# Performance work log

Hardware: AMD Instinct MI355X
Metric: run time of the kernel (lower is better)

The kernel has to match this reference:

```python
import jax, jax.numpy as jnp
import numpy as np

B, T, D_MODEL, H, RPR_K = 2, 2048, 1024, 16, 8
DK = D_MODEL // H  # 64
NUM_RPR = 2 * RPR_K + 1


def setup_inputs() -> dict:
    key = jax.random.key(0)
    ks = jax.random.split(key, 16)
    s = 0.02
    inp = {
        "query": jax.random.normal(ks[0], (B, T, D_MODEL), jnp.float32),
        "key": jax.random.normal(ks[1], (B, T, D_MODEL), jnp.float32),
        "value": jax.random.normal(ks[2], (B, T, D_MODEL), jnp.float32),
        "mask": jnp.ones((B, 1, 1, T), dtype=bool),
        "w_q": jax.random.normal(ks[3], (D_MODEL, H * DK), jnp.float32) * s,
        "b_q": jnp.zeros((H * DK,), jnp.float32),
        "w_k": jax.random.normal(ks[4], (D_MODEL, H * DK), jnp.float32) * s,
        "b_k": jnp.zeros((H * DK,), jnp.float32),
        "w_v": jax.random.normal(ks[5], (D_MODEL, H * DK), jnp.float32) * s,
        "b_v": jnp.zeros((H * DK,), jnp.float32),
        "w_o": jax.random.normal(ks[6], (H * DK, D_MODEL), jnp.float32) * s,
        "b_o": jnp.zeros((D_MODEL,), jnp.float32),
        "rpr_key_table": jax.random.normal(ks[7], (NUM_RPR, DK), jnp.float32),
        "rpr_value_table": jax.random.normal(ks[8], (NUM_RPR, DK), jnp.float32),
    }
    return inp


def _rel_edges(seq_len):
    # edges[i, j] = clamp(j - i + rpr_k, 0, 2*rpr_k)  -> [T, T] int32
    seq = jnp.arange(seq_len)
    edges = seq[None, :] - seq[:, None] + RPR_K
    return jnp.clip(edges, 0, 2 * RPR_K)


def reference(query, key, value, mask, w_q, b_q, w_k, b_k, w_v, b_v,
              w_o, b_o, rpr_key_table, rpr_value_table):
    Bsz, Tlen, _ = query.shape
    edges = _rel_edges(Tlen)                       # [T, T]
    ek = rpr_key_table[edges]                      # [T, T, DK]
    ev = rpr_value_table[edges]                    # [T, T, DK]

    def proj(x, w, b):
        return (x @ w + b).reshape(Bsz, Tlen, H, DK).transpose(0, 2, 1, 3)  # [B,H,T,DK]

    q = proj(query, w_q, b_q)
    k = proj(key, w_k, b_k)
    v = proj(value, w_v, b_v)

    scores_qk = jnp.einsum('bhtd,bhsd->bhts', q, k)
    scores_qek = jnp.einsum('bhtd,tsd->bhts', q, ek)
    scores = (scores_qk + scores_qek) / jnp.sqrt(jnp.float32(DK))
    scores = jnp.where(mask, scores, jnp.float32(-1e9))
    a = jax.nn.softmax(scores, axis=-1)            # [B,H,T,T]

    upd = jnp.einsum('bhts,bhsd->bhtd', a, v)
    upd_e = jnp.einsum('bhts,tsd->bhtd', a, ev)
    x = (upd + upd_e).transpose(0, 2, 1, 3).reshape(Bsz, Tlen, H * DK)
    return x @ w_o + b_o
```

## Files before the change

### kernel.cpp

```cpp
#include <hip/hip_runtime.h>
#include <stdint.h>


typedef unsigned short u16;
typedef __attribute__((ext_vector_type(4))) float f32x4;
typedef __attribute__((ext_vector_type(16))) float f32x16;
typedef __attribute__((ext_vector_type(4))) int   i32x4;
typedef __attribute__((ext_vector_type(8))) __bf16 bh8;

#define T_LEN 2048
#define NHEAD 16
#define NR    17

#define SCALE_LOG2 0.18033688011112042f

#define AW15_OFF 0
#define LA_OFF   1048576
#define A0_OFF   1114112
#define A16_OFF  1179648
#define LB_OFF   1245184

__device__ __forceinline__ float bf2f(u16 x) {
  unsigned u = ((unsigned)x) << 16;
  return __builtin_bit_cast(float, u);
}
__device__ __forceinline__ u16 f2bf(float f) {
  unsigned u = __builtin_bit_cast(unsigned, f);
  u = u + 0x7fffu + ((u >> 16) & 1u);
  return (u16)(u >> 16);
}
__device__ __forceinline__ f32x4 zero4() { f32x4 z = {0.f, 0.f, 0.f, 0.f}; return z; }
__device__ __forceinline__ f32x16 zero16() {
  f32x16 z = {0.f, 0.f, 0.f, 0.f, 0.f, 0.f, 0.f, 0.f,
              0.f, 0.f, 0.f, 0.f, 0.f, 0.f, 0.f, 0.f};
  return z;
}

__device__ __forceinline__ f32x4 mfma16(bh8 a, bh8 b, f32x4 c) {
  return __builtin_amdgcn_mfma_f32_16x16x32_bf16(a, b, c, 0, 0, 0);
}
__device__ __forceinline__ f32x16 mfma32(bh8 a, bh8 b, f32x16 c) {
  return __builtin_amdgcn_mfma_f32_32x32x16_bf16(a, b, c, 0, 0, 0);
}

__device__ __forceinline__ unsigned cvtpk(float a, float b) {
  unsigned r;
  asm("v_cvt_pk_bf16_f32 %0, %1, %2" : "=v"(r) : "v"(a), "v"(b));
  return r;
}

__device__ __forceinline__ void bar_sync() {
  __builtin_amdgcn_sched_barrier(0);
  asm volatile("s_waitcnt lgkmcnt(0)" ::: "memory");
  __builtin_amdgcn_s_barrier();
  __builtin_amdgcn_sched_barrier(0);
}

__device__ __forceinline__ void wait_vm0() {
  __builtin_amdgcn_sched_barrier(0);
  asm volatile("s_waitcnt vmcnt(0)" ::: "memory");
  __builtin_amdgcn_sched_barrier(0);
}

__device__ __forceinline__ void async16(const u16* g, u16* l) {
  __builtin_amdgcn_global_load_lds(
      (const __attribute__((address_space(1))) void*)g,
      (__attribute__((address_space(3))) void*)l, 16, 0, 0);
}

__device__ __forceinline__ bh8 ldfrag(const u16* base, int row, int qc) {
  const i32x4 v = *(const i32x4*)(base + row * 64 + ((qc ^ (row & 7)) << 3));
  return __builtin_bit_cast(bh8, v);
}

__global__ __launch_bounds__(256) void prep_kernel(
    const float* __restrict__ xq, const float* __restrict__ xk,
    const float* __restrict__ xv, const float* __restrict__ w0,
    const float* __restrict__ w1, const float* __restrict__ w2,
    const float* __restrict__ w3, u16* __restrict__ oq, u16* __restrict__ ok,
    u16* __restrict__ ov, u16* __restrict__ t0, u16* __restrict__ t1,
    u16* __restrict__ t2, u16* __restrict__ t3) {
  __shared__ u16 tile[32][33];
  const int z = blockIdx.z;
  if (z < 3) {
    const float* S = (z == 0) ? xq : (z == 1) ? xk : xv;
    u16* D = (z == 0) ? oq : (z == 1) ? ok : ov;
    const size_t i = ((size_t)blockIdx.x * 256 + threadIdx.x) * 8;
    const f32x4 v0 = *(const f32x4*)(S + i);
    const f32x4 v1 = *(const f32x4*)(S + i + 4);
    u16 o[8];
#pragma unroll
    for (int j = 0; j < 4; ++j) {
      o[j] = f2bf(v0[j]);
      o[4 + j] = f2bf(v1[j]);
    }
    i32x4 w;
    __builtin_memcpy(&w, o, 16);
    *(i32x4*)(D + i) = w;
  } else {
    if (blockIdx.x >= 1024) return;
    const float* S = (z == 3) ? w0 : (z == 4) ? w1 : (z == 5) ? w2 : w3;
    u16* D = (z == 3) ? t0 : (z == 4) ? t1 : (z == 5) ? t2 : t3;
    const int tx = threadIdx.x & 31, ty = threadIdx.x >> 5;
    const int bx = blockIdx.x & 31, by = blockIdx.x >> 5;
#pragma unroll
    for (int i = 0; i < 4; ++i) {
      const int y = by * 32 + ty + i * 8;
      tile[ty + i * 8][tx] = f2bf(S[(size_t)y * 1024 + bx * 32 + tx]);
    }
    __syncthreads();
#pragma unroll
    for (int i = 0; i < 4; ++i) {
      const int y = bx * 32 + ty + i * 8;
      D[(size_t)y * 1024 + by * 32 + tx] = tile[tx][ty + i * 8];
    }
  }
}

__device__ __forceinline__ void gemm_body(const u16* __restrict__ A,
                                          const u16* __restrict__ Bm,
                                          const float* __restrict__ bias,
                                          void* __restrict__ out, int mode,
                                          int bm, int bn, float oscale) {
  __shared__ __align__(16) u16 As[2][128 * 32];
  __shared__ __align__(16) u16 Bs[2][128 * 32];
  const int tid = threadIdx.x;
  const int wv = tid >> 6;
  const int ln = tid & 63;
  const int quad = ln >> 4, l15 = ln & 15;
  const int wr = wv >> 1, wc = wv & 1;

  f32x4 acc[4][4];
#pragma unroll
  for (int i = 0; i < 4; ++i)
#pragma unroll
    for (int j = 0; j < 4; ++j) acc[i][j] = zero4();

  const int c0 = tid, c1 = tid + 256;
  const size_t aoff0 = (size_t)(bm * 128 + (c0 >> 2)) * 1024 + (c0 & 3) * 8;
  const size_t aoff1 = (size_t)(bm * 128 + (c1 >> 2)) * 1024 + (c1 & 3) * 8;
  const size_t boff0 = (size_t)(bn * 128 + (c0 >> 2)) * 1024 + (c0 & 3) * 8;
  const size_t boff1 = (size_t)(bn * 128 + (c1 >> 2)) * 1024 + (c1 & 3) * 8;

  u16* ad0[2] = {&As[0][(wv * 64) * 8], &As[1][(wv * 64) * 8]};
  u16* ad1[2] = {&As[0][(256 + wv * 64) * 8], &As[1][(256 + wv * 64) * 8]};
  u16* bd0[2] = {&Bs[0][(wv * 64) * 8], &Bs[1][(wv * 64) * 8]};
  u16* bd1[2] = {&Bs[0][(256 + wv * 64) * 8], &Bs[1][(256 + wv * 64) * 8]};

  async16(A + aoff0, ad0[0]);
  async16(A + aoff1, ad1[0]);
  async16(Bm + boff0, bd0[0]);
  async16(Bm + boff1, bd1[0]);
  __syncthreads();

  for (int kt = 0; kt < 32; ++kt) {
    const int cur = kt & 1, nxt = cur ^ 1;
    if (kt < 31) {
      const int ko = (kt + 1) * 32;
      async16(A + aoff0 + ko, ad0[nxt]);
      async16(A + aoff1 + ko, ad1[nxt]);
      async16(Bm + boff0 + ko, bd0[nxt]);
      async16(Bm + boff1 + ko, bd1[nxt]);
    }

    bh8 af[4], bf[4];
#pragma unroll
    for (int mi = 0; mi < 4; ++mi)
      af[mi] = __builtin_bit_cast(
          bh8,
          *(const i32x4*)&As[cur][(wr * 64 + mi * 16 + l15) * 32 + quad * 8]);
#pragma unroll
    for (int ni = 0; ni < 4; ++ni)
      bf[ni] = __builtin_bit_cast(
          bh8,
          *(const i32x4*)&Bs[cur][(wc * 64 + ni * 16 + l15) * 32 + quad * 8]);
#pragma unroll
    for (int mi = 0; mi < 4; ++mi)
#pragma unroll
      for (int ni = 0; ni < 4; ++ni)
        acc[mi][ni] = mfma16(af[mi], bf[ni], acc[mi][ni]);

    __syncthreads();
  }

#pragma unroll
  for (int mi = 0; mi < 4; ++mi) {
    const int row0 = bm * 128 + wr * 64 + mi * 16 + quad * 4;
#pragma unroll
    for (int ni = 0; ni < 4; ++ni) {
      const int col = bn * 128 + wc * 64 + ni * 16 + l15;
      const float bcol = (mode == 3) ? 0.f : bias[col];
#pragma unroll
      for (int reg = 0; reg < 4; ++reg) {
        const int r = row0 + reg;
        const float v = acc[mi][ni][reg] + ((mode == 3) ? bias[r] : bcol);
        if (mode == 1) {
          const int bb = r >> 11, t = r & 2047;
          const int h = col >> 6, d = col & 63;
          ((u16*)out)[(((size_t)bb * NHEAD + h) * T_LEN + (size_t)t) * 64 + d] =
              f2bf(v * oscale);
        } else {
          const int h = r >> 6, d = r & 63;
          const int bb = col >> 11, t = col & 2047;
          ((u16*)out)[(((size_t)bb * NHEAD + h) * 64 + (size_t)d) * T_LEN + t] =
              f2bf(v);
        }
      }
    }
  }
}

__global__ __launch_bounds__(256) void gemm_qkv_kernel(
    const u16* __restrict__ xq, const u16* __restrict__ xk,
    const u16* __restrict__ xv, const u16* __restrict__ wtq,
    const u16* __restrict__ wtk, const u16* __restrict__ wtv,
    const float* __restrict__ bq, const float* __restrict__ bk,
    const float* __restrict__ bv, u16* __restrict__ oq, u16* __restrict__ ok,
    u16* __restrict__ ovt) {
  const int z = blockIdx.z;
  if (z == 0)
    gemm_body(xq, wtq, bq, oq, 1, blockIdx.x, blockIdx.y, SCALE_LOG2);
  else if (z == 1)
    gemm_body(xk, wtk, bk, ok, 1, blockIdx.x, blockIdx.y, 1.f);
  else
    gemm_body(wtv, xv, bv, ovt, 3, blockIdx.y, blockIdx.x, 1.f);
}

__global__ __launch_bounds__(256) void gemm_o_kernel(const u16* __restrict__ Ublk,
                                                     const u16* __restrict__ Bm,
                                                     const float* __restrict__ bias,
                                                     float* __restrict__ out) {
  __shared__ __align__(16) u16 As[2][64 * 32];
  __shared__ __align__(16) u16 Bs[2][128 * 32];
  const int tid = threadIdx.x;
  const int wv = tid >> 6;
  const int ln = tid & 63;
  const int quad = ln >> 4, l15 = ln & 15;
  const int wr = wv >> 1, wc = wv & 1;
  const int bm = blockIdx.x, bn = blockIdx.y;

  f32x4 acc[2][4];
#pragma unroll
  for (int i = 0; i < 2; ++i)
#pragma unroll
    for (int j = 0; j < 4; ++j) acc[i][j] = zero4();

  const int c0 = tid, c1 = tid + 256;
  const int rA = bm * 64 + (c0 >> 2);
  const int tA = rA & 2047, bbA = rA >> 11;
  const size_t abase = (size_t)(tA >> 7);
  const size_t boff0 = (size_t)(bn * 128 + (c0 >> 2)) * 1024 + (c0 & 3) * 8;
  const size_t boff1 = (size_t)(bn * 128 + (c1 >> 2)) * 1024 + (c1 & 3) * 8;

  u16* ad0[2] = {&As[0][(wv * 64) * 8], &As[1][(wv * 64) * 8]};
  u16* bd0[2] = {&Bs[0][(wv * 64) * 8], &Bs[1][(wv * 64) * 8]};
  u16* bd1[2] = {&Bs[0][(256 + wv * 64) * 8], &Bs[1][(256 + wv * 64) * 8]};

  auto aoff = [&](int kt) -> size_t {
    const int c = kt * 32 + (c0 & 3) * 8;
    const int h = c >> 6, d = c & 63;
    const size_t idx = (size_t)(bbA * 16 + h) * 16 + abase;
    return idx * 16384 + (size_t)(tA & 127) * 64 + d;
  };

  async16(Ublk + aoff(0), ad0[0]);
  async16(Bm + boff0, bd0[0]);
  async16(Bm + boff1, bd1[0]);
  __syncthreads();

  for (int kt = 0; kt < 32; ++kt) {
    const int cur = kt & 1, nxt = cur ^ 1;
    if (kt < 31) {
      const int ko = (kt + 1) * 32;
      async16(Ublk + aoff(kt + 1), ad0[nxt]);
      async16(Bm + boff0 + ko, bd0[nxt]);
      async16(Bm + boff1 + ko, bd1[nxt]);
    }

    bh8 af[2], bf[4];
#pragma unroll
    for (int mi = 0; mi < 2; ++mi)
      af[mi] = __builtin_bit_cast(
          bh8,
          *(const i32x4*)&As[cur][(wr * 32 + mi * 16 + l15) * 32 + quad * 8]);
#pragma unroll
    for (int ni = 0; ni < 4; ++ni)
      bf[ni] = __builtin_bit_cast(
          bh8,
          *(const i32x4*)&Bs[cur][(wc * 64 + ni * 16 + l15) * 32 + quad * 8]);
#pragma unroll
    for (int mi = 0; mi < 2; ++mi)
#pragma unroll
      for (int ni = 0; ni < 4; ++ni)
        acc[mi][ni] = mfma16(af[mi], bf[ni], acc[mi][ni]);

    __syncthreads();
  }

#pragma unroll
  for (int mi = 0; mi < 2; ++mi) {
    const int row0 = bm * 64 + wr * 32 + mi * 16 + quad * 4;
#pragma unroll
    for (int ni = 0; ni < 4; ++ni) {
      const int col = bn * 128 + wc * 64 + ni * 16 + l15;
      const float bcol = bias[col];
#pragma unroll
      for (int reg = 0; reg < 4; ++reg)
        out[(size_t)(row0 + reg) * 1024 + col] = acc[mi][ni][reg] + bcol;
    }
  }
}

__global__ __launch_bounds__(256, 3) void attn_kernel(
    const u16* __restrict__ Qw, const u16* __restrict__ Kw,
    const u16* __restrict__ Vtw, const float* __restrict__ rkt,
    float* __restrict__ Oa, float* __restrict__ ObLo, float* __restrict__ ObHi,
    float* __restrict__ awb) {
  __shared__ __align__(16) u16 smu[16384];
  __shared__ float smf[4096];
  u16* const Qs = smu;
  float* const qes = smf;
  float* const aw15 = smf + 2176;

  const int tid = threadIdx.x;
  const int wv = tid >> 6, ln = tid & 63;
  const int l31 = ln & 31, hi = ln >> 5;
  const int wg = blockIdx.x;
  const int xcd = wg & 7;
  const int rest = wg >> 3;
  const int sh = rest >> 6;
  const int sub = rest & 63;
  const int qt = sub & 15;
  const int bh = xcd * 4 + (sub >> 4);
  const int idx = bh * 16 + qt;
  const size_t hb = (size_t)bh * (T_LEN * 64);
  const int t0 = qt * 128 + wv * 32;
  const int tl = wv * 32 + l31;

  const int cut = (2 * qt + 3 > 32) ? 32 : (2 * qt + 3);
  const int stBeg = sh ? cut : 0;
  const int stEnd = sh ? 32 : cut;

  float* const opart = (sh == 0)
                           ? (Oa + (size_t)idx * 8192)
                           : (idx < 256 ? ObLo + (size_t)idx * 8192
                                        : ObHi + (size_t)(idx - 256) * 8192);

  if (stBeg >= stEnd) {
    for (int i = tid; i < 8192; i += 256) opart[i] = 0.f;
    if (tid < 128) awb[LB_OFF + idx * 128 + tid] = 0.f;
    return;
  }

  const int r8 = ln >> 3, c8 = ln & 7;
  const int kgp = c8 ^ (r8 & 7);
  const u16* ksrc0 = Kw + hb + (size_t)(wv * 16 + r8) * 64 + kgp * 8;
  const u16* ksrc1 = Kw + hb + (size_t)(wv * 16 + 8 + r8) * 64 + kgp * 8;
  const u16* vsrc0 = Vtw + hb + (size_t)(wv * 16 + r8) * T_LEN + kgp * 8;
  const u16* vsrc1 = Vtw + hb + (size_t)(wv * 16 + 8 + r8) * T_LEN + kgp * 8;
  u16* const ldsK0 = smu + (wv * 16) * 64;
  u16* const ldsK1 = smu + (wv * 16 + 8) * 64;
  u16* const ldsV0 = smu + 8192 + (wv * 16) * 64;
  u16* const ldsV1 = smu + 8192 + (wv * 16 + 8) * 64;

  {
    const u16* qsrc = Qw + hb + (size_t)(qt * 128 + wv * 32 + r8) * 64 + kgp * 8;
#pragma unroll
    for (int a = 0; a < 4; ++a)
      async16(qsrc + (size_t)(a * 8) * 64, Qs + (wv * 32 + a * 8) * 64);
  }
  wait_vm0();
  bar_sync();

  if (sh == 0) {
    for (int i = tid; i < 128 * NR; i += 256) {
      const int row = i / NR, r = i - row * NR;
      float s = 0.f;
#pragma unroll
      for (int c = 0; c < 8; ++c) {
        const i32x4 qv = *(const i32x4*)&Qs[row * 64 + ((c ^ (row & 7)) << 3)];
        const u16* qq = (const u16*)&qv;
#pragma unroll
        for (int j = 0; j < 8; ++j) s += bf2f(qq[j]) * rkt[r * 64 + c * 8 + j];
      }
      qes[i] = s;
    }
    for (int i = tid; i < 128 * 15; i += 256) aw15[i] = 0.f;
  } else {
    for (int row = tid; row < 128; row += 256) {
      float s = 0.f;
#pragma unroll
      for (int c = 0; c < 8; ++c) {
        const i32x4 qv = *(const i32x4*)&Qs[row * 64 + ((c ^ (row & 7)) << 3)];
        const u16* qq = (const u16*)&qv;
#pragma unroll
        for (int j = 0; j < 8; ++j)
          s += bf2f(qq[j]) * rkt[16 * 64 + c * 8 + j];
      }
      qes[row * NR + 16] = s;
    }
  }
  bar_sync();

  const float qb0 = (sh == 0) ? qes[tl * NR + 0] : 0.f;
  const float qb16 = qes[tl * NR + 16];
  bh8 qf[4];
#pragma unroll
  for (int kb = 0; kb < 4; ++kb) qf[kb] = ldfrag(Qs, tl, kb * 2 + hi);
  bar_sync();

  {
    const int b0 = stBeg & 1;
    async16(ksrc0 + (size_t)stBeg * 4096, ldsK0 + b0 * 4096);
    async16(ksrc1 + (size_t)stBeg * 4096, ldsK1 + b0 * 4096);
    async16(vsrc0 + (size_t)stBeg * 64, ldsV0 + b0 * 4096);
    async16(vsrc1 + (size_t)stBeg * 64, ldsV1 + b0 * 4096);
  }
  wait_vm0();
  bar_sync();

  float l_l = 0.f, s0_l = 0.f, s16_l = 0.f;
  f32x16 oacc[2] = {zero16(), zero16()};

  for (int st = stBeg; st < stEnd; ++st) {
    const int cur = st & 1;
    const u16* Kc = smu + cur * 4096;
    const u16* Vc = smu + 8192 + cur * 4096;
    if (st + 1 < stEnd) {
      const int nxt = cur ^ 1;
      async16(ksrc0 + (size_t)(st + 1) * 4096, ldsK0 + nxt * 4096);
      async16(ksrc1 + (size_t)(st + 1) * 4096, ldsK1 + nxt * 4096);
      async16(vsrc0 + (size_t)(st + 1) * 64, ldsV0 + nxt * 4096);
      async16(vsrc1 + (size_t)(st + 1) * 64, ldsV1 + nxt * 4096);
    }
    __builtin_amdgcn_s_setprio(1);

#pragma unroll
    for (int sb = 0; sb < 2; ++sb) {
      f32x16 sacc = zero16();
#pragma unroll
      for (int kb = 0; kb < 4; ++kb) {
        const bh8 kf = ldfrag(Kc, sb * 32 + l31, kb * 2 + hi);
        sacc = mfma32(kf, qf[kb], sacc);
      }

      const int sbase = st * 64 + sb * 32;
      float p[16];
      if (sbase + 39 <= t0) {
        float ts = 0.f;
#pragma unroll
        for (int r = 0; r < 16; ++r) {
          const float pv = __builtin_amdgcn_exp2f(sacc[r] + qb0);
          p[r] = pv;
          ts += pv;
        }
        l_l += ts;
        s0_l += ts;
      } else if (sbase >= t0 + 39) {
        float ts = 0.f;
#pragma unroll
        for (int r = 0; r < 16; ++r) {
          const float pv = __builtin_amdgcn_exp2f(sacc[r] + qb16);
          p[r] = pv;
          ts += pv;
        }
        l_l += ts;
        s16_l += ts;
      } else {
        const int base = sbase + 4 * hi - (t0 + l31) + 8;
#pragma unroll
        for (int r = 0; r < 16; ++r) {
          int rel = base + (r & 3) + 8 * (r >> 2);
          rel = rel < 0 ? 0 : (rel > 16 ? 16 : rel);
          const float pv =
              __builtin_amdgcn_exp2f(sacc[r] + qes[tl * NR + rel]);
          p[r] = pv;
          l_l += pv;
          if (rel == 0)
            s0_l += pv;
          else if (rel == 16)
            s16_l += pv;
          else
            atomicAdd(&aw15[tl * 15 + rel - 1], pv);
        }
      }

#pragma unroll
      for (int h = 0; h < 2; ++h) {
        unsigned wa = cvtpk(p[8 * h + 0], p[8 * h + 1]);
        unsigned wb = cvtpk(p[8 * h + 2], p[8 * h + 3]);
        unsigned wc = cvtpk(p[8 * h + 4], p[8 * h + 5]);
        unsigned wd = cvtpk(p[8 * h + 6], p[8 * h + 7]);
        asm("v_permlane32_swap_b32 %0, %1" : "+v"(wa), "+v"(wc));
        asm("v_permlane32_swap_b32 %0, %1" : "+v"(wb), "+v"(wd));
        const i32x4 fr = {(int)wa, (int)wb, (int)wc, (int)wd};
        const bh8 pa = __builtin_bit_cast(bh8, fr);
        const int ks = sb * 2 + h;
#pragma unroll
        for (int db = 0; db < 2; ++db) {
          const bh8 vf = ldfrag(Vc, db * 32 + l31, ks * 2 + hi);
          oacc[db] = mfma32(pa, vf, oacc[db]);
        }
      }
    }
    __builtin_amdgcn_s_setprio(0);

    wait_vm0();
    bar_sync();
  }

  l_l += __shfl_xor(l_l, 32);
  s0_l += __shfl_xor(s0_l, 32);
  s16_l += __shfl_xor(s16_l, 32);
  if (sh == 0) {
    if (ln < 32) {
      awb[LA_OFF + idx * 128 + tl] = l_l;
      awb[A0_OFF + idx * 128 + tl] = s0_l;
      awb[A16_OFF + idx * 128 + tl] = s16_l;
    }
  } else {
    if (ln < 32) awb[LB_OFF + idx * 128 + tl] = l_l;
  }

#pragma unroll
  for (int r = 0; r < 16; ++r) {
    const int srow = (r & 3) + 8 * (r >> 2) + 4 * hi;
    const int trow = wv * 32 + srow;
    opart[trow * 64 + l31] = oacc[0][r];
    opart[trow * 64 + 32 + l31] = oacc[1][r];
  }

  if (sh == 0) {
    __syncthreads();
    for (int i = tid; i < 128 * 15; i += 256)
      awb[AW15_OFF + (size_t)idx * 1920 + i] = aw15[i];
  }
}

__global__ __launch_bounds__(256) void combine_kernel(
    const float* __restrict__ Oa, const float* __restrict__ ObLo,
    const float* __restrict__ ObHi, const float* __restrict__ awb,
    const float* __restrict__ rvt, u16* __restrict__ Ublk) {
  __shared__ float os[8192];
  __shared__ float rvs[NR * 64];
  const int tid = threadIdx.x;
  const int idx = blockIdx.x;
  const float* oa = Oa + (size_t)idx * 8192;
  const float* ob = (idx < 256) ? ObLo + (size_t)idx * 8192
                                : ObHi + (size_t)(idx - 256) * 8192;
  for (int i = tid; i < 8192; i += 256) os[i] = oa[i] + ob[i];
  for (int i = tid; i < NR * 64; i += 256) rvs[i] = rvt[i];
  __syncthreads();

  const int row = tid >> 1, d0 = (tid & 1) * 32;
  const float lB = awb[LB_OFF + idx * 128 + row];
  const float linv = 1.f / (awb[LA_OFF + idx * 128 + row] + lB);
  const float a0 = awb[A0_OFF + idx * 128 + row];
  const float a16 = awb[A16_OFF + idx * 128 + row] + lB;
  float aw[15];
#pragma unroll
  for (int r = 0; r < 15; ++r)
    aw[r] = awb[AW15_OFF + (size_t)idx * 1920 + row * 15 + r];

#pragma unroll 4
  for (int j = 0; j < 32; ++j) {
    const int d = d0 + j;
    float e = a0 * rvs[d] + a16 * rvs[16 * 64 + d];
#pragma unroll
    for (int r = 1; r < 16; ++r) e += aw[r - 1] * rvs[r * 64 + d];
    const float u = (os[row * 64 + d] + e) * linv;
    Ublk[(size_t)idx * 16384 + row * 64 + d] = f2bf(u);
  }
}

extern "C" void kernel_launch(void* const* d_in, const int* in_sizes, int n_in,
                              void* d_out, int out_size, void* d_ws,
                              size_t ws_size, hipStream_t stream) {
  const float* query = (const float*)d_in[0];
  const float* key = (const float*)d_in[1];
  const float* value = (const float*)d_in[2];
  const float* w_q = (const float*)d_in[4];
  const float* b_q = (const float*)d_in[5];
  const float* w_k = (const float*)d_in[6];
  const float* b_k = (const float*)d_in[7];
  const float* w_v = (const float*)d_in[8];
  const float* b_v = (const float*)d_in[9];
  const float* w_o = (const float*)d_in[10];
  const float* b_o = (const float*)d_in[11];
  const float* rkt = (const float*)d_in[12];
  const float* rvt = (const float*)d_in[13];

  char* ws = (char*)d_ws;
  const size_t MB = 1u << 20;
  u16* wtq = (u16*)(ws + 0 * MB);
  u16* wtk = (u16*)(ws + 2 * MB);
  u16* wtv = (u16*)(ws + 4 * MB);
  u16* wto = (u16*)(ws + 6 * MB);
  u16* Xq = (u16*)(ws + 8 * MB);
  u16* Xk = (u16*)(ws + 16 * MB);
  u16* Xv = (u16*)(ws + 24 * MB);
  u16* Qw = (u16*)(ws + 32 * MB);
  u16* Kw = (u16*)(ws + 40 * MB);
  u16* Vtw = (u16*)(ws + 48 * MB);
  u16* Uw = (u16*)(ws + 56 * MB);
  float* Oa = (float*)(ws + 8 * MB);
  float* ObLo = (float*)(ws + 24 * MB);
  float* ObHi = (float*)(ws + 56 * MB);
  float* awb = (float*)(ws + 0 * MB);
  u16* Ublk = (u16*)(ws + 8 * MB);

  prep_kernel<<<dim3(2048, 1, 7), 256, 0, stream>>>(
      query, key, value, w_q, w_k, w_v, w_o, Xq, Xk, Xv, wtq, wtk, wtv, wto);
  gemm_qkv_kernel<<<dim3(32, 8, 3), 256, 0, stream>>>(
      Xq, Xk, Xv, wtq, wtk, wtv, b_q, b_k, b_v, Qw, Kw, Vtw);
  attn_kernel<<<dim3(1024), 256, 0, stream>>>(Qw, Kw, Vtw, rkt, Oa, ObLo,
                                              ObHi, awb);
  combine_kernel<<<dim3(512), 256, 0, stream>>>(Oa, ObLo, ObHi, awb, rvt,
                                                Ublk);
  gemm_o_kernel<<<dim3(64, 8), 256, 0, stream>>>(Ublk, wto, b_o,
                                                 (float*)d_out);
}
```

Baseline: 282.4 us.

## Split attention KV range evenly and reduce partials with atomics

Attention work is now split into two equal halves of the key range per query tile instead of an uneven causal-style cut, and the partial outputs and band weights are combined with atomicAdd into a zeroed buffer rather than separate per-half buffers. Combine reads one accumulator and writes U in row-major token layout, so gemm_o can use plain strided A loads. The QKV and output GEMM grids are remapped to 1D with XCD-aware tile ordering for better L2 locality. This adds two memsets and atomic traffic, and the second half now recomputes all rpr-key dot products.

Result: slower. 323.7 us (+14.6%).

```diff
diff --git a/kernel.cpp b/kernel.cpp
--- a/kernel.cpp
+++ b/kernel.cpp
@@ -14,11 +14,10 @@
 
 #define SCALE_LOG2 0.18033688011112042f
 
-#define AW15_OFF 0
-#define LA_OFF   1048576
-#define A0_OFF   1114112
-#define A16_OFF  1179648
-#define LB_OFF   1245184
+#define AW15G_OFF 0
+#define LBASE     1048576
+#define A0BASE    1179648
+#define A16BASE   1310720
 
 __device__ __forceinline__ float bf2f(u16 x) {
   unsigned u = ((unsigned)x) << 16;
@@ -217,16 +216,19 @@
     const float* __restrict__ bq, const float* __restrict__ bk,
     const float* __restrict__ bv, u16* __restrict__ oq, u16* __restrict__ ok,
     u16* __restrict__ ovt) {
-  const int z = blockIdx.z;
+  const int wg = blockIdx.x;
+  const int xcd = wg & 7, bn = (wg >> 3) & 7, bmh = (wg >> 6) & 3;
+  const int z = wg >> 8;
+  const int bm = bmh * 8 + xcd;
   if (z == 0)
-    gemm_body(xq, wtq, bq, oq, 1, blockIdx.x, blockIdx.y, SCALE_LOG2);
+    gemm_body(xq, wtq, bq, oq, 1, bm, bn, SCALE_LOG2);
   else if (z == 1)
-    gemm_body(xk, wtk, bk, ok, 1, blockIdx.x, blockIdx.y, 1.f);
+    gemm_body(xk, wtk, bk, ok, 1, bm, bn, 1.f);
   else
-    gemm_body(wtv, xv, bv, ovt, 3, blockIdx.y, blockIdx.x, 1.f);
-}
-
-__global__ __launch_bounds__(256) void gemm_o_kernel(const u16* __restrict__ Ublk,
+    gemm_body(wtv, xv, bv, ovt, 3, bn, bm, 1.f);
+}
+
+__global__ __launch_bounds__(256) void gemm_o_kernel(const u16* __restrict__ A,
                                                      const u16* __restrict__ Bm,
                                                      const float* __restrict__ bias,
                                                      float* __restrict__ out) {
@@ -237,7 +239,9 @@
   const int ln = tid & 63;
   const int quad = ln >> 4, l15 = ln & 15;
   const int wr = wv >> 1, wc = wv & 1;
-  const int bm = blockIdx.x, bn = blockIdx.y;
+  const int wg = blockIdx.x;
+  const int xcd = wg & 7, bn = (wg >> 3) & 7, bmh = wg >> 6;
+  const int bm = bmh * 8 + xcd;
 
   f32x4 acc[2][4];
 #pragma unroll
@@ -246,9 +250,7 @@
     for (int j = 0; j < 4; ++j) acc[i][j] = zero4();
 
   const int c0 = tid, c1 = tid + 256;
-  const int rA = bm * 64 + (c0 >> 2);
-  const int tA = rA & 2047, bbA = rA >> 11;
-  const size_t abase = (size_t)(tA >> 7);
+  const size_t aoff0 = (size_t)(bm * 64 + (c0 >> 2)) * 1024 + (c0 & 3) * 8;
   const size_t boff0 = (size_t)(bn * 128 + (c0 >> 2)) * 1024 + (c0 & 3) * 8;
   const size_t boff1 = (size_t)(bn * 128 + (c1 >> 2)) * 1024 + (c1 & 3) * 8;
 
@@ -256,14 +258,7 @@
   u16* bd0[2] = {&Bs[0][(wv * 64) * 8], &Bs[1][(wv * 64) * 8]};
   u16* bd1[2] = {&Bs[0][(256 + wv * 64) * 8], &Bs[1][(256 + wv * 64) * 8]};
 
-  auto aoff = [&](int kt) -> size_t {
-    const int c = kt * 32 + (c0 & 3) * 8;
-    const int h = c >> 6, d = c & 63;
-    const size_t idx = (size_t)(bbA * 16 + h) * 16 + abase;
-    return idx * 16384 + (size_t)(tA & 127) * 64 + d;
-  };
-
-  async16(Ublk + aoff(0), ad0[0]);
+  async16(A + aoff0, ad0[0]);
   async16(Bm + boff0, bd0[0]);
   async16(Bm + boff1, bd1[0]);
   __syncthreads();
@@ -272,7 +267,7 @@
     const int cur = kt & 1, nxt = cur ^ 1;
     if (kt < 31) {
       const int ko = (kt + 1) * 32;
-      async16(Ublk + aoff(kt + 1), ad0[nxt]);
+      async16(A + aoff0 + ko, ad0[nxt]);
       async16(Bm + boff0 + ko, bd0[nxt]);
       async16(Bm + boff1 + ko, bd1[nxt]);
     }
@@ -314,8 +309,7 @@
 __global__ __launch_bounds__(256, 3) void attn_kernel(
     const u16* __restrict__ Qw, const u16* __restrict__ Kw,
     const u16* __restrict__ Vtw, const float* __restrict__ rkt,
-    float* __restrict__ Oa, float* __restrict__ ObLo, float* __restrict__ ObHi,
-    float* __restrict__ awb) {
+    float* __restrict__ Oacc, float* __restrict__ awb) {
   __shared__ __align__(16) u16 smu[16384];
   __shared__ float smf[4096];
   u16* const Qs = smu;
@@ -327,30 +321,16 @@
   const int l31 = ln & 31, hi = ln >> 5;
   const int wg = blockIdx.x;
   const int xcd = wg & 7;
-  const int rest = wg >> 3;
-  const int sh = rest >> 6;
-  const int sub = rest & 63;
-  const int qt = sub & 15;
-  const int bh = xcd * 4 + (sub >> 4);
+  const int qt = (wg >> 3) & 15;
+  const int bhl = (wg >> 7) & 3;
+  const int sh = wg >> 9;
+  const int bh = xcd * 4 + bhl;
   const int idx = bh * 16 + qt;
   const size_t hb = (size_t)bh * (T_LEN * 64);
   const int t0 = qt * 128 + wv * 32;
   const int tl = wv * 32 + l31;
 
-  const int cut = (2 * qt + 3 > 32) ? 32 : (2 * qt + 3);
-  const int stBeg = sh ? cut : 0;
-  const int stEnd = sh ? 32 : cut;
-
-  float* const opart = (sh == 0)
-                           ? (Oa + (size_t)idx * 8192)
-                           : (idx < 256 ? ObLo + (size_t)idx * 8192
-                                        : ObHi + (size_t)(idx - 256) * 8192);
-
-  if (stBeg >= stEnd) {
-    for (int i = tid; i < 8192; i += 256) opart[i] = 0.f;
-    if (tid < 128) awb[LB_OFF + idx * 128 + tid] = 0.f;
-    return;
-  }
+  const int stBeg = sh * 16, stEnd = stBeg + 16;
 
   const int r8 = ln >> 3, c8 = ln & 7;
   const int kgp = c8 ^ (r8 & 7);
@@ -372,37 +352,22 @@
   wait_vm0();
   bar_sync();
 
-  if (sh == 0) {
-    for (int i = tid; i < 128 * NR; i += 256) {
-      const int row = i / NR, r = i - row * NR;
-      float s = 0.f;
-#pragma unroll
-      for (int c = 0; c < 8; ++c) {
-        const i32x4 qv = *(const i32x4*)&Qs[row * 64 + ((c ^ (row & 7)) << 3)];
-        const u16* qq = (const u16*)&qv;
-#pragma unroll
-        for (int j = 0; j < 8; ++j) s += bf2f(qq[j]) * rkt[r * 64 + c * 8 + j];
-      }
-      qes[i] = s;
-    }
-    for (int i = tid; i < 128 * 15; i += 256) aw15[i] = 0.f;
-  } else {
-    for (int row = tid; row < 128; row += 256) {
-      float s = 0.f;
-#pragma unroll
-      for (int c = 0; c < 8; ++c) {
-        const i32x4 qv = *(const i32x4*)&Qs[row * 64 + ((c ^ (row & 7)) << 3)];
-        const u16* qq = (const u16*)&qv;
-#pragma unroll
-        for (int j = 0; j < 8; ++j)
-          s += bf2f(qq[j]) * rkt[16 * 64 + c * 8 + j];
-      }
-      qes[row * NR + 16] = s;
-    }
-  }
+  for (int i = tid; i < 128 * NR; i += 256) {
+    const int row = i / NR, r = i - row * NR;
+    float s = 0.f;
+#pragma unroll
+    for (int c = 0; c < 8; ++c) {
+      const i32x4 qv = *(const i32x4*)&Qs[row * 64 + ((c ^ (row & 7)) << 3)];
+      const u16* qq = (const u16*)&qv;
+#pragma unroll
+      for (int j = 0; j < 8; ++j) s += bf2f(qq[j]) * rkt[r * 64 + c * 8 + j];
+    }
+    qes[i] = s;
+  }
+  for (int i = tid; i < 128 * 15; i += 256) aw15[i] = 0.f;
   bar_sync();
 
-  const float qb0 = (sh == 0) ? qes[tl * NR + 0] : 0.f;
+  const float qb0 = qes[tl * NR + 0];
   const float qb16 = qes[tl * NR + 16];
   bh8 qf[4];
 #pragma unroll
@@ -512,64 +477,63 @@
   l_l += __shfl_xor(l_l, 32);
   s0_l += __shfl_xor(s0_l, 32);
   s16_l += __shfl_xor(s16_l, 32);
-  if (sh == 0) {
-    if (ln < 32) {
-      awb[LA_OFF + idx * 128 + tl] = l_l;
-      awb[A0_OFF + idx * 128 + tl] = s0_l;
-      awb[A16_OFF + idx * 128 + tl] = s16_l;
-    }
-  } else {
-    if (ln < 32) awb[LB_OFF + idx * 128 + tl] = l_l;
-  }
-
+  if (ln < 32) {
+    awb[LBASE + sh * 65536 + idx * 128 + tl] = l_l;
+    awb[A0BASE + sh * 65536 + idx * 128 + tl] = s0_l;
+    awb[A16BASE + sh * 65536 + idx * 128 + tl] = s16_l;
+  }
+
+  float* const obase = Oacc + (size_t)idx * 8192;
 #pragma unroll
   for (int r = 0; r < 16; ++r) {
     const int srow = (r & 3) + 8 * (r >> 2) + 4 * hi;
     const int trow = wv * 32 + srow;
-    opart[trow * 64 + l31] = oacc[0][r];
-    opart[trow * 64 + 32 + l31] = oacc[1][r];
-  }
-
-  if (sh == 0) {
-    __syncthreads();
-    for (int i = tid; i < 128 * 15; i += 256)
-      awb[AW15_OFF + (size_t)idx * 1920 + i] = aw15[i];
+    atomicAdd(&obase[trow * 64 + l31], oacc[0][r]);
+    atomicAdd(&obase[trow * 64 + 32 + l31], oacc[1][r]);
+  }
+
+  __syncthreads();
+  for (int i = tid; i < 128 * 15; i += 256) {
+    const float v = aw15[i];
+    if (v != 0.f) atomicAdd(&awb[AW15G_OFF + (size_t)idx * 1920 + i], v);
   }
 }
 
 __global__ __launch_bounds__(256) void combine_kernel(
-    const float* __restrict__ Oa, const float* __restrict__ ObLo,
-    const float* __restrict__ ObHi, const float* __restrict__ awb,
-    const float* __restrict__ rvt, u16* __restrict__ Ublk) {
+    const float* __restrict__ Oacc, const float* __restrict__ awb,
+    const float* __restrict__ rvt, u16* __restrict__ U) {
   __shared__ float os[8192];
   __shared__ float rvs[NR * 64];
   const int tid = threadIdx.x;
-  const int idx = blockIdx.x;
-  const float* oa = Oa + (size_t)idx * 8192;
-  const float* ob = (idx < 256) ? ObLo + (size_t)idx * 8192
-                                : ObHi + (size_t)(idx - 256) * 8192;
-  for (int i = tid; i < 8192; i += 256) os[i] = oa[i] + ob[i];
+  const int wg = blockIdx.x;
+  const int idx = (wg & 7) * 64 + (wg >> 3);
+  const float* oa = Oacc + (size_t)idx * 8192;
+  for (int i = tid; i < 8192; i += 256) os[i] = oa[i];
   for (int i = tid; i < NR * 64; i += 256) rvs[i] = rvt[i];
   __syncthreads();
 
   const int row = tid >> 1, d0 = (tid & 1) * 32;
-  const float lB = awb[LB_OFF + idx * 128 + row];
-  const float linv = 1.f / (awb[LA_OFF + idx * 128 + row] + lB);
-  const float a0 = awb[A0_OFF + idx * 128 + row];
-  const float a16 = awb[A16_OFF + idx * 128 + row] + lB;
+  const float lsum = awb[LBASE + idx * 128 + row] +
+                     awb[LBASE + 65536 + idx * 128 + row];
+  const float linv = 1.f / lsum;
+  const float a0 = awb[A0BASE + idx * 128 + row] +
+                   awb[A0BASE + 65536 + idx * 128 + row];
+  const float a16 = awb[A16BASE + idx * 128 + row] +
+                    awb[A16BASE + 65536 + idx * 128 + row];
   float aw[15];
 #pragma unroll
   for (int r = 0; r < 15; ++r)
-    aw[r] = awb[AW15_OFF + (size_t)idx * 1920 + row * 15 + r];
-
+    aw[r] = awb[AW15G_OFF + (size_t)idx * 1920 + row * 15 + r];
+
+  const int qt = idx & 15, h = (idx >> 4) & 15, bb = idx >> 8;
+  const size_t ubase = ((size_t)bb * T_LEN + qt * 128 + row) * 1024 + h * 64;
 #pragma unroll 4
   for (int j = 0; j < 32; ++j) {
     const int d = d0 + j;
     float e = a0 * rvs[d] + a16 * rvs[16 * 64 + d];
 #pragma unroll
     for (int r = 1; r < 16; ++r) e += aw[r - 1] * rvs[r * 64 + d];
-    const float u = (os[row * 64 + d] + e) * linv;
-    Ublk[(size_t)idx * 16384 + row * 64 + d] = f2bf(u);
+    U[ubase + d] = f2bf((os[row * 64 + d] + e) * linv);
   }
 }
 
@@ -603,20 +567,16 @@
   u16* Kw = (u16*)(ws + 40 * MB);
   u16* Vtw = (u16*)(ws + 48 * MB);
   u16* Uw = (u16*)(ws + 56 * MB);
-  float* Oa = (float*)(ws + 8 * MB);
-  float* ObLo = (float*)(ws + 24 * MB);
-  float* ObHi = (float*)(ws + 56 * MB);
+  float* Oacc = (float*)(ws + 8 * MB);
   float* awb = (float*)(ws + 0 * MB);
-  u16* Ublk = (u16*)(ws + 8 * MB);
 
   prep_kernel<<<dim3(2048, 1, 7), 256, 0, stream>>>(
       query, key, value, w_q, w_k, w_v, w_o, Xq, Xk, Xv, wtq, wtk, wtv, wto);
-  gemm_qkv_kernel<<<dim3(32, 8, 3), 256, 0, stream>>>(
+  gemm_qkv_kernel<<<dim3(768), 256, 0, stream>>>(
       Xq, Xk, Xv, wtq, wtk, wtv, b_q, b_k, b_v, Qw, Kw, Vtw);
-  attn_kernel<<<dim3(1024), 256, 0, stream>>>(Qw, Kw, Vtw, rkt, Oa, ObLo,
-                                              ObHi, awb);
-  combine_kernel<<<dim3(512), 256, 0, stream>>>(Oa, ObLo, ObHi, awb, rvt,
-                                                Ublk);
-  gemm_o_kernel<<<dim3(64, 8), 256, 0, stream>>>(Ublk, wto, b_o,
-                                                 (float*)d_out);
-}
+  hipMemsetAsync(Oacc, 0, (size_t)16 * MB, stream);
+  hipMemsetAsync(awb, 0, (size_t)983040 * 4, stream);
+  attn_kernel<<<dim3(1024), 256, 0, stream>>>(Qw, Kw, Vtw, rkt, Oacc, awb);
+  combine_kernel<<<dim3(512), 256, 0, stream>>>(Oacc, awb, rvt, Uw);
+  gemm_o_kernel<<<dim3(512), 256, 0, stream>>>(Uw, wto, b_o, (float*)d_out);
+}
```
